# Optimization experiments

Hardware: AMD Instinct MI355X
Metric: run time of the kernel (lower is better)

## Reference

```python
import math
import jax, jax.numpy as jnp
import numpy as np

B, T, C = 4, 2048, 1024
H = 16
HS = C // H  # head_size = 64

def setup_inputs() -> dict:
    key = jax.random.key(0)
    k1, k2, k3 = jax.random.split(key, 3)
    x = jax.random.normal(k1, (B, T, C), dtype=jnp.float32)
    W_qkv = jax.random.normal(k2, (C, 3 * C), dtype=jnp.float32) * (1.0 / math.sqrt(C))
    W_proj = jax.random.normal(k3, (C, C), dtype=jnp.float32) * (1.0 / math.sqrt(C))
    b_proj = jnp.zeros((C,), dtype=jnp.float32)
    return {"x": x, "W_qkv": W_qkv, "W_proj": W_proj, "b_proj": b_proj}

def reference(x, W_qkv, W_proj, b_proj):
    Bx, Tx, Cx = x.shape
    qkv = x @ W_qkv  # [B,T,3C]
    q, k, v = jnp.split(qkv, 3, axis=-1)
    # [B,T,C] -> [B,H,T,HS]
    def heads(t):
        return t.reshape(Bx, Tx, H, HS).transpose(0, 2, 1, 3)
    q, k, v = heads(q), heads(k), heads(v)
    scores = jnp.einsum('bhqd,bhkd->bhqk', q, k) / math.sqrt(HS)
    causal = jnp.tril(jnp.ones((Tx, Tx), dtype=bool))
    scores = jnp.where(causal, scores, -jnp.inf)
    attn = jax.nn.softmax(scores, axis=-1)
    out = jnp.einsum('bhqk,bhkd->bhqd', attn, v)  # [B,H,T,HS]
    out = out.transpose(0, 2, 1, 3).reshape(Bx, Tx, Cx)
    return out @ W_proj + b_proj
```

## Files before the change

kernel.cpp:

```cpp
#include <hip/hip_runtime.h>
#include <hip/hip_bf16.h>
#include <cstdint>
#include <cstddef>

using bf16 = __hip_bfloat16;
typedef __attribute__((ext_vector_type(8))) short short8;
typedef __attribute__((ext_vector_type(4))) float floatx4;

#define B_ 4
#define T_ 2048
#define C_ 1024
#define H_ 16
#define HS_ 64
#define BT_ (B_*T_)
#define N3C (3*C_)

#define MFMA16(a,b,c) __builtin_amdgcn_mfma_f32_16x16x32_bf16((a),(b),(c),0,0,0)

#if __has_builtin(__builtin_amdgcn_exp2f)
#define EXP2(x) __builtin_amdgcn_exp2f(x)
#else
#define EXP2(x) exp2f(x)
#endif

static __device__ __forceinline__ void gld16(const bf16* g, bf16* l) {
  __builtin_amdgcn_global_load_lds(
      (const __attribute__((address_space(1))) unsigned int*)g,
      (__attribute__((address_space(3))) unsigned int*)l, 16, 0, 0);
}

static __device__ __forceinline__ unsigned short f2bf_us(float x) {
  bf16 b = __float2bfloat16(x);
  return *(unsigned short*)&b;
}

__global__ __launch_bounds__(256)
void k_prep(const float* __restrict__ x, bf16* __restrict__ xb,
            const float* __restrict__ Wqkv, bf16* __restrict__ wqkvT,
            const float* __restrict__ Wproj, bf16* __restrict__ wprojT)
{
  const int bid = blockIdx.x, tid = threadIdx.x;
  __shared__ float tile[64][65];

  if (bid < 8192) {
    const int i = bid*256 + tid;
    float4 v = ((const float4*)x)[i];
    union { bf16 b[4]; uint2 u; } cvt;
    cvt.b[0] = __float2bfloat16(v.x);
    cvt.b[1] = __float2bfloat16(v.y);
    cvt.b[2] = __float2bfloat16(v.z);
    cvt.b[3] = __float2bfloat16(v.w);
    ((uint2*)xb)[i] = cvt.u;
    return;
  }

  const float* in; bf16* out; int N, n0, k0;
  if (bid < 8960) {
    const int j = bid - 8192;
    in = Wqkv; out = wqkvT; N = N3C;
    n0 = (j % 48) * 64; k0 = (j / 48) * 64;
  } else {
    const int j = bid - 8960;
    in = Wproj; out = wprojT; N = C_;
    n0 = (j % 16) * 64; k0 = (j / 16) * 64;
  }
  const int r = tid >> 6, c = tid & 63;
  #pragma unroll
  for (int j = 0; j < 16; ++j)
    tile[r + j*4][c] = in[(size_t)(k0 + r + j*4) * N + n0 + c];
  __syncthreads();
  #pragma unroll
  for (int j = 0; j < 16; ++j) {
    int rr = r + j*4;
    out[(size_t)(n0 + rr) * C_ + k0 + c] = __float2bfloat16(tile[c][rr]);
  }
}

template<int MODE, int NB>
__global__ __launch_bounds__(256, 2)
void k_gemm(const bf16* __restrict__ A, const bf16* __restrict__ Bt,
            int N, int K,
            bf16* __restrict__ Qb, bf16* __restrict__ Kb, bf16* __restrict__ Vt,
            float* __restrict__ Out, const float* __restrict__ bias)
{
  __shared__ __align__(16) char smem[33856];
  bf16* const sAb = (bf16*)smem;
  bf16* const sBb = (bf16*)(smem + 16384);

  const int tid  = threadIdx.x;
  const int lane = tid & 63, wave = tid >> 6;
  const int quad = lane >> 4, l16 = lane & 15;
  const int wm = wave >> 1, wn = wave & 1;

  const int g = blockIdx.x;
  const int xcd = g & 7;
  const int local = g >> 3;
  const int nb = local % NB;
  const int mb = (local / NB) * 8 + xcd;
  const int m0 = mb * 128, n0 = nb * 128;

  const int ra = tid >> 2;
  const int gc = (tid & 3) ^ ((ra >> 1) & 3);
  const bf16* aptr = A  + (size_t)(m0 + ra) * K + gc*8;
  const bf16* bptr = Bt + (size_t)(n0 + ra) * K + gc*8;
  const size_t rowjump = (size_t)64 * K;

  floatx4 acc[4][4] = {};
  const int KI = K >> 5;
  const int pc = quad ^ ((l16 >> 1) & 3);

  for (int i = 0; i <= KI; ++i) {
    __syncthreads();
    if (i < KI) {
      const int k0 = i << 5;
      bf16* sa = sAb + (i & 1) * 4096;
      bf16* sb = sBb + (i & 1) * 4096;
      gld16(aptr + k0,           sa + tid*8);
      gld16(aptr + rowjump + k0, sa + 2048 + tid*8);
      gld16(bptr + k0,           sb + tid*8);
      gld16(bptr + rowjump + k0, sb + 2048 + tid*8);
    }
    if (i == 0) continue;
    const bf16* sa = sAb + ((i-1) & 1) * 4096;
    const bf16* sb = sBb + ((i-1) & 1) * 4096;
    short8 af[4], bfm[4];
    #pragma unroll
    for (int ii = 0; ii < 4; ++ii)
      af[ii] = *(const short8*)&sa[(wm*64 + ii*16 + l16) * 32 + pc*8];
    #pragma unroll
    for (int ii = 0; ii < 4; ++ii)
      bfm[ii] = *(const short8*)&sb[(wn*64 + ii*16 + l16) * 32 + pc*8];
    #pragma unroll
    for (int ii = 0; ii < 4; ++ii)
      #pragma unroll
      for (int j = 0; j < 4; ++j)
        acc[ii][j] = MFMA16(af[ii], bfm[j], acc[ii][j]);
  }

  if (MODE == 0 && nb >= 16) {
    __syncthreads();
    unsigned short* epi = (unsigned short*)smem;
    #pragma unroll
    for (int i = 0; i < 4; ++i) {
      const int tl = wm*64 + i*16 + quad*4;
      #pragma unroll
      for (int j = 0; j < 4; ++j) {
        const int ccl = wn*64 + j*16 + l16;
        #pragma unroll
        for (int r = 0; r < 4; ++r)
          epi[ccl*132 + tl + r] = f2bf_us(acc[i][j][r]);
      }
    }
    __syncthreads();
    const int b  = m0 >> 11;
    const int t0 = m0 & 2047;
    const int h0 = (n0 - 2*C_) >> 6;
    #pragma unroll
    for (int it = 0; it < 32; ++it) {
      const int id = it*256 + tid;
      const int tp = id & 31;
      const int rest = id >> 5;
      const int tl64 = (rest & 1) * 64;
      const int ccl = rest >> 1;
      const int k0p = tp + (tp & 16);
      const unsigned lo = epi[ccl*132 + tl64 + k0p];
      const unsigned hi = epi[ccl*132 + tl64 + k0p + 16];
      const int h = h0 + (ccl >> 6), d = ccl & 63;
      unsigned* row = (unsigned*)(Vt + ((size_t)(b*H_ + h) * HS_ + d) * T_);
      row[(t0 >> 1) + tl64/2 + tp] = lo | (hi << 16);
    }
  } else {
    #pragma unroll
    for (int i = 0; i < 4; ++i) {
      const int rowb = m0 + wm*64 + i*16 + quad*4;
      #pragma unroll
      for (int j = 0; j < 4; ++j) {
        const int col = n0 + wn*64 + j*16 + l16;
        #pragma unroll
        for (int r = 0; r < 4; ++r) {
          const float v = acc[i][j][r];
          const int rr = rowb + r;
          if (MODE == 0) {
            const int b = rr >> 11, t = rr & 2047;
            const int h = (col >> 6) & 15, d = col & 63;
            const size_t addr = (((size_t)(b*H_ + h) * T_ + t) << 6) + d;
            if (nb < 8) {
              Qb[addr] = __float2bfloat16(v * 0.18033688f);
            } else {
              Kb[addr] = __float2bfloat16(v);
            }
          } else {
            Out[(size_t)rr * N + col] = v + bias[col];
          }
        }
      }
    }
  }
}

__global__ __launch_bounds__(256, 2)
void k_attn(const bf16* __restrict__ Q, const bf16* __restrict__ K,
            const bf16* __restrict__ Vt, bf16* __restrict__ att)
{
  __shared__ bf16 kbuf[2][64*64];
  __shared__ bf16 vbuf[2][64*64];
  __shared__ bf16 pbuf[4][32*64];

  const int tid  = threadIdx.x;
  const int lane = tid & 63, wave = tid >> 6;
  const int quad = lane >> 4, l16 = lane & 15;
  const int x7 = l16 & 7;

  const int g  = blockIdx.x;
  const int bh = (g & 7) * 8 + (g >> 6);
  const int bx = (g >> 3) & 7;
  const int b = bh >> 4, h = bh & 15;

  const bf16* Qp = Q  + (size_t)bh * T_ * HS_;
  const bf16* Kp = K  + (size_t)bh * T_ * HS_;
  const bf16* Vp = Vt + (size_t)bh * HS_ * T_;

  const int qbase[2] = { (15-bx)*128 + wave*32, bx*128 + wave*32 };
  const int ntk0 = 32 - 2*bx;
  const int ntk1 = 2*bx + 2;

  short8 qf[2][2][2];
  #pragma unroll
  for (int t = 0; t < 2; ++t)
    #pragma unroll
    for (int mt = 0; mt < 2; ++mt)
      #pragma unroll
      for (int ss = 0; ss < 2; ++ss)
        qf[t][mt][ss] = *(const short8*)(Qp + (size_t)(qbase[t] + mt*16 + l16) * HS_ + ss*32 + quad*8);

  floatx4 o[2][2][4] = {};
  float lrow[2][2][4] = {};

  const bf16* kg[2]; const bf16* vg[2];
  int ldsoff[2];
  #pragma unroll
  for (int it = 0; it < 2; ++it) {
    const int c = it*256 + tid;
    const int row = c >> 3;
    const int col = (c & 7) ^ (row & 7);
    kg[it] = Kp + (size_t)row * HS_ + col*8;
    vg[it] = Vp + (size_t)row * T_ + col*8;
    ldsoff[it] = c*8;
  }

  bf16* pw = pbuf[wave];
  unsigned int* pw32 = (unsigned int*)pw;
  const int c0 = l16 >> 2;
  const int dwl = l16 & 3;

  for (int i = 0; i <= ntk0; ++i) {
    __syncthreads();
    if (i < ntk0) {
      const int stk0 = i * 64;
      bf16* kb = kbuf[i & 1];
      bf16* vb = vbuf[i & 1];
      #pragma unroll
      for (int it = 0; it < 2; ++it) {
        gld16(kg[it] + (size_t)stk0 * HS_, kb + ldsoff[it]);
        gld16(vg[it] + stk0,               vb + ldsoff[it]);
      }
    }
    if (i == 0) continue;
    const int tk  = i - 1;
    const int tk0 = tk * 64;
    const bf16* kb = kbuf[tk & 1];
    const bf16* vb = vbuf[tk & 1];

    #pragma unroll
    for (int t = 0; t < 2; ++t) {
      if (t == 1 && tk >= ntk1) break;
      if (tk0 > qbase[t] + 31) continue;

      floatx4 s[2][4] = {};
      #pragma unroll
      for (int nt = 0; nt < 4; ++nt) {
        const int key = nt*16 + l16;
        #pragma unroll
        for (int ss = 0; ss < 2; ++ss) {
          short8 kf = *(const short8*)&kb[(key*8 + ((ss*4+quad) ^ x7))*8];
          s[0][nt] = MFMA16(qf[t][0][ss], kf, s[0][nt]);
          s[1][nt] = MFMA16(qf[t][1][ss], kf, s[1][nt]);
        }
      }

      if (tk0 + 63 > qbase[t]) {
        #pragma unroll
        for (int mt = 0; mt < 2; ++mt)
          #pragma unroll
          for (int nt = 0; nt < 4; ++nt) {
            const int key = tk0 + nt*16 + l16;
            #pragma unroll
            for (int r = 0; r < 4; ++r) {
              const int qr = qbase[t] + mt*16 + quad*4 + r;
              if (key > qr) s[mt][nt][r] = -1e30f;
            }
          }
      }

      #pragma unroll
      for (int mt = 0; mt < 2; ++mt) {
        #pragma unroll
        for (int r = 0; r < 4; ++r) {
          const float p0 = EXP2(s[mt][0][r]), p1 = EXP2(s[mt][1][r]);
          const float p2 = EXP2(s[mt][2][r]), p3 = EXP2(s[mt][3][r]);
          lrow[t][mt][r] += (p0 + p1) + (p2 + p3);
          const int q = mt*16 + quad*4 + r;
          const unsigned w0 = __builtin_amdgcn_perm(__float_as_uint(p1), __float_as_uint(p0), 0x07060302u);
          const unsigned w1 = __builtin_amdgcn_perm(__float_as_uint(p3), __float_as_uint(p2), 0x07060302u);
          pw32[q*32 + (((c0 + q)     & 7) << 2) + dwl] = w0;
          pw32[q*32 + (((c0 + q + 4) & 7) << 2) + dwl] = w1;
        }
      }

      #pragma unroll
      for (int ss = 0; ss < 2; ++ss) {
        short8 pf0 = *(const short8*)&pw[l16*64      + ((4*ss + quad + l16) & 7)*8];
        short8 pf1 = *(const short8*)&pw[(16+l16)*64 + ((4*ss + quad + l16) & 7)*8];
        #pragma unroll
        for (int nd = 0; nd < 4; ++nd) {
          const int d = nd*16 + l16;
          short8 vf = *(const short8*)&vb[(d*8 + ((ss*4+quad) ^ x7))*8];
          o[t][0][nd] = MFMA16(pf0, vf, o[t][0][nd]);
          o[t][1][nd] = MFMA16(pf1, vf, o[t][1][nd]);
        }
      }
    }
  }

  #pragma unroll
  for (int t = 0; t < 2; ++t) {
    #pragma unroll
    for (int mt = 0; mt < 2; ++mt) {
      #pragma unroll
      for (int r = 0; r < 4; ++r) {
        float lsum = lrow[t][mt][r];
        lsum += __shfl_xor(lsum, 1);
        lsum += __shfl_xor(lsum, 2);
        lsum += __shfl_xor(lsum, 4);
        lsum += __shfl_xor(lsum, 8);
        const float inv = 1.0f / lsum;
        const int tt = qbase[t] + mt*16 + quad*4 + r;
        #pragma unroll
        for (int nd = 0; nd < 4; ++nd)
          att[(size_t)(b*T_ + tt) * C_ + h*64 + nd*16 + l16] =
              __float2bfloat16(o[t][mt][nd][r] * inv);
      }
    }
  }
}

extern "C" void kernel_launch(void* const* d_in, const int* in_sizes, int n_in,
                              void* d_out, int out_size, void* d_ws, size_t ws_size,
                              hipStream_t stream) {
  const float* x     = (const float*)d_in[0];
  const float* Wqkv  = (const float*)d_in[1];
  const float* Wproj = (const float*)d_in[2];
  const float* bproj = (const float*)d_in[3];
  float* out = (float*)d_out;

  char* ws = (char*)d_ws;
  bf16* xb     = (bf16*)(ws + 0);
  bf16* wqkvT  = (bf16*)(ws + 16777216);
  bf16* wprojT = (bf16*)(ws + 23068672);
  bf16* Qb     = (bf16*)(ws + 25165824);
  bf16* Kb     = (bf16*)(ws + 41943040);
  bf16* Vt     = (bf16*)(ws + 58720256);
  bf16* att    = (bf16*)(ws + 75497472);

  k_prep<<<dim3(9216), 256, 0, stream>>>(x, xb, Wqkv, wqkvT, Wproj, wprojT);
  k_gemm<0, 24><<<dim3(1536), 256, 0, stream>>>(
      xb, wqkvT, N3C, C_, Qb, Kb, Vt, nullptr, nullptr);
  k_attn<<<dim3(512), 256, 0, stream>>>(Qb, Kb, Vt, att);
  k_gemm<1, 8><<<dim3(512), 256, 0, stream>>>(
      att, wprojT, C_, C_, nullptr, nullptr, nullptr, out, bproj);
}
```

Baseline: 237.6 us.

## Double GEMM K-tile to 64 with 8-way XOR swizzle; widen x conversion

The GEMM K-step goes from 32 to 64. Each stage now loads 128x64 tiles of A and B through four 16-byte global-to-LDS loads per thread, uses an 8-chunk XOR swizzle, and runs two MFMA sub-steps per barrier. This halves the number of __syncthreads and loop iterations per GEMM. The cost is LDS use doubling to 64KB per block, which may limit the two-blocks-per-CU occupancy target. The prep kernel also converts 8 floats per thread instead of 4, halving its block count for the x conversion.

```diff
diff --git a/kernel.cpp b/kernel.cpp
--- a/kernel.cpp
+++ b/kernel.cpp
@@ -42,25 +42,30 @@
   const int bid = blockIdx.x, tid = threadIdx.x;
   __shared__ float tile[64][65];
 
-  if (bid < 8192) {
+  if (bid < 4096) {
     const int i = bid*256 + tid;
-    float4 v = ((const float4*)x)[i];
-    union { bf16 b[4]; uint2 u; } cvt;
-    cvt.b[0] = __float2bfloat16(v.x);
-    cvt.b[1] = __float2bfloat16(v.y);
-    cvt.b[2] = __float2bfloat16(v.z);
-    cvt.b[3] = __float2bfloat16(v.w);
-    ((uint2*)xb)[i] = cvt.u;
+    const float4 v0 = ((const float4*)x)[2*i];
+    const float4 v1 = ((const float4*)x)[2*i + 1];
+    union { bf16 b[8]; uint4 u; } cvt;
+    cvt.b[0] = __float2bfloat16(v0.x);
+    cvt.b[1] = __float2bfloat16(v0.y);
+    cvt.b[2] = __float2bfloat16(v0.z);
+    cvt.b[3] = __float2bfloat16(v0.w);
+    cvt.b[4] = __float2bfloat16(v1.x);
+    cvt.b[5] = __float2bfloat16(v1.y);
+    cvt.b[6] = __float2bfloat16(v1.z);
+    cvt.b[7] = __float2bfloat16(v1.w);
+    ((uint4*)xb)[i] = cvt.u;
     return;
   }
 
   const float* in; bf16* out; int N, n0, k0;
-  if (bid < 8960) {
-    const int j = bid - 8192;
+  if (bid < 4864) {
+    const int j = bid - 4096;
     in = Wqkv; out = wqkvT; N = N3C;
     n0 = (j % 48) * 64; k0 = (j / 48) * 64;
   } else {
-    const int j = bid - 8960;
+    const int j = bid - 4864;
     in = Wproj; out = wprojT; N = C_;
     n0 = (j % 16) * 64; k0 = (j / 16) * 64;
   }
@@ -83,9 +88,9 @@
             bf16* __restrict__ Qb, bf16* __restrict__ Kb, bf16* __restrict__ Vt,
             float* __restrict__ Out, const float* __restrict__ bias)
 {
-  __shared__ __align__(16) char smem[33856];
+  __shared__ __align__(16) char smem[65536];
   bf16* const sAb = (bf16*)smem;
-  bf16* const sBb = (bf16*)(smem + 16384);
+  bf16* const sBb = (bf16*)(smem + 32768);
 
   const int tid  = threadIdx.x;
   const int lane = tid & 63, wave = tid >> 6;
@@ -99,42 +104,46 @@
   const int mb = (local / NB) * 8 + xcd;
   const int m0 = mb * 128, n0 = nb * 128;
 
-  const int ra = tid >> 2;
-  const int gc = (tid & 3) ^ ((ra >> 1) & 3);
+  const int ra = tid >> 3;
+  const int gc = (tid & 7) ^ (ra & 7);
   const bf16* aptr = A  + (size_t)(m0 + ra) * K + gc*8;
   const bf16* bptr = Bt + (size_t)(n0 + ra) * K + gc*8;
-  const size_t rowjump = (size_t)64 * K;
+  const size_t rj = (size_t)32 * K;
 
   floatx4 acc[4][4] = {};
-  const int KI = K >> 5;
-  const int pc = quad ^ ((l16 >> 1) & 3);
+  const int KI = K >> 6;
+  const int x7a = l16 & 7;
 
   for (int i = 0; i <= KI; ++i) {
     __syncthreads();
     if (i < KI) {
-      const int k0 = i << 5;
-      bf16* sa = sAb + (i & 1) * 4096;
-      bf16* sb = sBb + (i & 1) * 4096;
-      gld16(aptr + k0,           sa + tid*8);
-      gld16(aptr + rowjump + k0, sa + 2048 + tid*8);
-      gld16(bptr + k0,           sb + tid*8);
-      gld16(bptr + rowjump + k0, sb + 2048 + tid*8);
+      const int k0 = i << 6;
+      bf16* sa = sAb + (i & 1) * 8192;
+      bf16* sb = sBb + (i & 1) * 8192;
+      #pragma unroll
+      for (int q2 = 0; q2 < 4; ++q2) {
+        gld16(aptr + q2*rj + k0, sa + q2*2048 + tid*8);
+        gld16(bptr + q2*rj + k0, sb + q2*2048 + tid*8);
+      }
     }
     if (i == 0) continue;
-    const bf16* sa = sAb + ((i-1) & 1) * 4096;
-    const bf16* sb = sBb + ((i-1) & 1) * 4096;
-    short8 af[4], bfm[4];
-    #pragma unroll
-    for (int ii = 0; ii < 4; ++ii)
-      af[ii] = *(const short8*)&sa[(wm*64 + ii*16 + l16) * 32 + pc*8];
-    #pragma unroll
-    for (int ii = 0; ii < 4; ++ii)
-      bfm[ii] = *(const short8*)&sb[(wn*64 + ii*16 + l16) * 32 + pc*8];
-    #pragma unroll
-    for (int ii = 0; ii < 4; ++ii)
-      #pragma unroll
-      for (int j = 0; j < 4; ++j)
-        acc[ii][j] = MFMA16(af[ii], bfm[j], acc[ii][j]);
+    const bf16* sa = sAb + ((i-1) & 1) * 8192;
+    const bf16* sb = sBb + ((i-1) & 1) * 8192;
+    #pragma unroll
+    for (int ks = 0; ks < 2; ++ks) {
+      short8 af[4], bfm[4];
+      #pragma unroll
+      for (int ii = 0; ii < 4; ++ii)
+        af[ii] = *(const short8*)&sa[(wm*64 + ii*16 + l16)*64 + ((ks*4 + quad) ^ x7a)*8];
+      #pragma unroll
+      for (int ii = 0; ii < 4; ++ii)
+        bfm[ii] = *(const short8*)&sb[(wn*64 + ii*16 + l16)*64 + ((ks*4 + quad) ^ x7a)*8];
+      #pragma unroll
+      for (int ii = 0; ii < 4; ++ii)
+        #pragma unroll
+        for (int j = 0; j < 4; ++j)
+          acc[ii][j] = MFMA16(af[ii], bfm[j], acc[ii][j]);
+    }
   }
 
   if (MODE == 0 && nb >= 16) {
@@ -372,7 +381,7 @@
   bf16* Vt     = (bf16*)(ws + 58720256);
   bf16* att    = (bf16*)(ws + 75497472);
 
-  k_prep<<<dim3(9216), 256, 0, stream>>>(x, xb, Wqkv, wqkvT, Wproj, wprojT);
+  k_prep<<<dim3(5120), 256, 0, stream>>>(x, xb, Wqkv, wqkvT, Wproj, wprojT);
   k_gemm<0, 24><<<dim3(1536), 256, 0, stream>>>(
       xb, wqkvT, N3C, C_, Qb, Kb, Vt, nullptr, nullptr);
   k_attn<<<dim3(512), 256, 0, stream>>>(Qb, Kb, Vt, att);
```

Result: faster. 221.1 us (-7.0%).
